# Kernel optimization log

Measured on AMD Instinct MI355X. Metric: run time of the kernel, lower is better.

Reference implementation:

```python
import jax, jax.numpy as jnp
import numpy as np

NUM_HEADS = 16
HEAD_DIM = 64  # latent_dim // num_heads = 1024 // 16


def setup_inputs() -> dict:
    key = jax.random.key(0)
    k1, k2, k3, k4 = jax.random.split(key, 4)
    B, S, C = 4, 2048, 1024
    x = jax.random.normal(k1, (B, S, C), dtype=jnp.float32)
    # torch nn.Linear weight layout: [out_features, in_features]
    W_qkv = jax.random.normal(k2, (2 * 1024 + C, C), dtype=jnp.float32) * (C ** -0.5)
    W_out = jax.random.normal(k3, (C, C), dtype=jnp.float32) * (C ** -0.5)
    b_out = jax.random.normal(k4, (C,), dtype=jnp.float32) * 0.01
    return {"x": x, "W_qkv": W_qkv, "W_out": W_out, "b_out": b_out}


def reference(x, W_qkv, W_out, b_out):
    B, S, C = x.shape
    H, CH = NUM_HEADS, HEAD_DIM
    qkv = jnp.einsum('bsc,oc->bso', x, W_qkv)          # [B, S, 2*latent + C]
    qkv = qkv.reshape(B, S, H, -1)                      # per-head: [CH, CH, C//H]
    q = qkv[..., :CH]
    k = qkv[..., CH:2 * CH]
    v = qkv[..., 2 * CH:]
    energy = jnp.einsum('bqhc,bkhc->bhqk', q, k)        # full score matrix
    scale = jnp.asarray(C, x.dtype) ** 0.5              # note: original scales by sqrt(C), not sqrt(head_dim)
    attn = jax.nn.softmax(energy / scale, axis=-1)
    out = jnp.einsum('bhqk,bkhc->bqhc', attn, v).reshape(B, S, -1)
    out = jnp.einsum('bsc,oc->bso', out, W_out) + b_out
    return out + x
```

## Files before the change

kernel.cpp:

```cpp
#include <hip/hip_runtime.h>
#include <hip/hip_bf16.h>
#include <stdint.h>

#define BB 4
#define SS 2048
#define CC 1024
#define HH 16
#define DD 64
#define MTOT (BB*SS)
#define NQKV 3072

typedef __attribute__((ext_vector_type(8))) short short8;
typedef __attribute__((ext_vector_type(4))) float f32x4;

#define MFMA16(A,B,C) __builtin_amdgcn_mfma_f32_16x16x32_bf16((A),(B),(C),0,0,0)
#define BARRIER() asm volatile("s_barrier" ::: "memory")

__device__ __forceinline__ ushort f2bf(float f) {
  uint32_t u = __builtin_bit_cast(uint32_t, f);
  u += 0x7FFFu + ((u >> 16) & 1u);
  return (ushort)(u >> 16);
}

__device__ __forceinline__ float bf2f(ushort u) {
  return __builtin_bit_cast(float, (uint32_t)u << 16);
}

__device__ __forceinline__ unsigned cvtpk(float lo, float hi) {
  unsigned r;
  asm("v_cvt_pk_bf16_f32 %0, %1, %2" : "=v"(r) : "v"(lo), "v"(hi));
  return r;
}

__device__ __forceinline__ float hw_exp2(float x) {
  float r;
  asm("v_exp_f32 %0, %1" : "=v"(r) : "v"(x));
  return r;
}

__global__ void cvt3_kernel(const float* __restrict__ a, ushort* __restrict__ da, int na4,
                            const float* __restrict__ b, ushort* __restrict__ db, int nb4,
                            const float* __restrict__ c, ushort* __restrict__ dc, int nc4) {
  int total = na4 + nb4 + nc4;
  int stride = gridDim.x * blockDim.x;
  for (int i = blockIdx.x * blockDim.x + threadIdx.x; i < total; i += stride) {
    const float4* s; ushort4* d; int k;
    if (i < na4)            { s = (const float4*)a; d = (ushort4*)da; k = i; }
    else if (i < na4 + nb4) { s = (const float4*)b; d = (ushort4*)db; k = i - na4; }
    else                    { s = (const float4*)c; d = (ushort4*)dc; k = i - na4 - nb4; }
    float4 v = s[k];
    ushort4 o;
    o.x = f2bf(v.x); o.y = f2bf(v.y); o.z = f2bf(v.z); o.w = f2bf(v.w);
    d[k] = o;
  }
}

__device__ __forceinline__ void stage_half128(const ushort* __restrict__ gsrc, ushort* ldsbase, int tid) {
  #pragma unroll
  for (int ld = 0; ld < 4; ++ld) {
    int ci = ld * 256 + tid;
    int row = ci >> 3, slot = ci & 7;
    const ushort* src = gsrc + (size_t)row * 1024 + ((slot ^ (row & 7)) << 3);
    __builtin_amdgcn_global_load_lds(
        (const __attribute__((address_space(1))) uint32_t*)src,
        (__attribute__((address_space(3))) uint32_t*)(ldsbase + ci * 8), 16, 0, 0);
  }
}

__device__ __forceinline__ short8 rd_frag(const ushort* Lb, int row, int slot) {
  return *(const short8*)(Lb + row * 64 + ((slot ^ (row & 7)) << 3));
}

__device__ __forceinline__ void core128(const ushort* __restrict__ A, const ushort* __restrict__ Bw,
                                        int m0, int n0, ushort* L, f32x4 acc[4][4]) {
  const int tid = threadIdx.x, lane = tid & 63, w = tid >> 6;
  const int q = lane & 15, g = lane >> 4;
  const int wm = (w >> 1) * 64, wn = (w & 1) * 64;
  const ushort* Ag = A + (size_t)m0 * 1024;
  const ushort* Bg = Bw + (size_t)n0 * 1024;

  #pragma unroll
  for (int tt = 0; tt < 2; ++tt) {
    stage_half128(Ag + tt * 64, L + tt * 16384, tid);
    stage_half128(Bg + tt * 64, L + tt * 16384 + 8192, tid);
  }
  asm volatile("s_waitcnt vmcnt(8)" ::: "memory");
  BARRIER();

  #pragma unroll 1
  for (int t = 0; t < 16; ++t) {
    const ushort* La = L + (t & 1) * 16384;
    const ushort* Lb = La + 8192;
    short8 af[4][2], bf[4][2];
    #pragma unroll
    for (int mi = 0; mi < 4; ++mi)
      #pragma unroll
      for (int ks = 0; ks < 2; ++ks)
        af[mi][ks] = rd_frag(La, wm + mi * 16 + q, ks * 4 + g);
    #pragma unroll
    for (int nj = 0; nj < 4; ++nj)
      #pragma unroll
      for (int ks = 0; ks < 2; ++ks)
        bf[nj][ks] = rd_frag(Lb, wn + nj * 16 + q, ks * 4 + g);
    #pragma unroll
    for (int mi = 0; mi < 4; ++mi)
      #pragma unroll
      for (int nj = 0; nj < 4; ++nj) {
        acc[mi][nj] = MFMA16(af[mi][0], bf[nj][0], acc[mi][nj]);
        acc[mi][nj] = MFMA16(af[mi][1], bf[nj][1], acc[mi][nj]);
      }
    BARRIER();
    if (t <= 13) {
      ushort* Ls = L + (t & 1) * 16384;
      stage_half128(Ag + (t + 2) * 64, Ls, tid);
      stage_half128(Bg + (t + 2) * 64, Ls + 8192, tid);
      asm volatile("s_waitcnt vmcnt(8)" ::: "memory");
      BARRIER();
    } else if (t == 14) {
      asm volatile("s_waitcnt vmcnt(0)" ::: "memory");
      BARRIER();
    }
  }
}

__global__ __launch_bounds__(256, 2) void gemm_qkv(const ushort* __restrict__ xb, const ushort* __restrict__ wqkv,
                                                   ushort* __restrict__ qfbuf, ushort* __restrict__ kfbuf,
                                                   ushort* __restrict__ vfbuf) {
  __shared__ __align__(16) ushort L[32768];
  const int bid = blockIdx.x;
  const int xcd = bid & 7, r0 = bid >> 3;
  const int m0 = (r0 / 3) * 128, n0 = (xcd * 3 + (r0 % 3)) * 128;

  f32x4 acc[4][4];
  #pragma unroll
  for (int i = 0; i < 4; ++i)
    #pragma unroll
    for (int j = 0; j < 4; ++j) acc[i][j] = f32x4{0.f, 0.f, 0.f, 0.f};
  core128(xb, wqkv, m0, n0, L, acc);

  const int lane = threadIdx.x & 63, wave = threadIdx.x >> 6;
  const int g = lane >> 4, q = lane & 15;
  const int wm = (wave >> 1) * 64, wn = (wave & 1) * 64;
  const int s0 = m0 & 2047, bb = m0 >> 11;

  #pragma unroll
  for (int j = 0; j < 4; ++j) {
    int n = n0 + wn + j * 16 + q;
    int h = n / 192;
    int which = (n - h * 192) >> 6;
    float scl = (which == 0) ? 0.045084222f : 1.0f;
    int nc = wn + j * 16 + q;
    #pragma unroll
    for (int i = 0; i < 4; ++i) {
      #pragma unroll
      for (int rr = 0; rr < 4; ++rr) {
        int mr = wm + i * 16 + g * 4 + rr;
        L[mr * 128 + (nc ^ ((mr & 7) << 4))] = f2bf(acc[i][j][rr] * scl);
      }
    }
  }
  __syncthreads();

  {
    const int n_g = n0 + wave * 32;
    const int h = n_g / 192, rem = n_g - h * 192, which = rem >> 6;
    const int bh = bb * 16 + h;
    if (which < 2) {
      ushort* dst0 = (which == 0) ? qfbuf : kfbuf;
      const int c0 = (rem & 63) >> 5;
      #pragma unroll
      for (int k = 0; k < 8; ++k) {
        int jt = (s0 >> 4) + k;
        int mr = k * 16 + (lane & 15);
        int nc0 = wave * 32 + (lane >> 4) * 8;
        short8 v = *(const short8*)(L + mr * 128 + (nc0 ^ ((mr & 7) << 4)));
        *(short8*)(dst0 + ((((size_t)bh * 128 + jt) * 2 + c0) * 64 + lane) * 8) = v;
      }
    } else {
      const int ct0 = (rem & 63) >> 4;
      #pragma unroll
      for (int k = 0; k < 8; ++k) {
        int jcr = k >> 1, ct = ct0 + (k & 1);
        int nc = wave * 32 + (k & 1) * 16 + (lane & 15);
        int mrb = jcr * 32 + (lane >> 4) * 8;
        short8 v;
        #pragma unroll
        for (int e = 0; e < 8; ++e) {
          int mr = mrb + e;
          v[e] = (short)L[mr * 128 + (nc ^ ((mr & 7) << 4))];
        }
        int jc = (s0 >> 5) + jcr;
        *(short8*)(vfbuf + ((((size_t)bh * 64 + jc) * 4 + ct) * 64 + lane) * 8) = v;
      }
    }
  }
}

__global__ __launch_bounds__(256, 2) void gemm_out(const ushort* __restrict__ ab, const ushort* __restrict__ wout,
                                                   const ushort* __restrict__ xbb, const float* __restrict__ bias,
                                                   float* __restrict__ out) {
  __shared__ __align__(16) ushort L[32768];
  const int bid = blockIdx.x;
  const int sw = (bid & 7) * 64 + (bid >> 3);
  const int m0 = (sw & 63) * 128, n0 = (sw >> 6) * 128;

  f32x4 acc[4][4];
  #pragma unroll
  for (int i = 0; i < 4; ++i)
    #pragma unroll
    for (int j = 0; j < 4; ++j) acc[i][j] = f32x4{0.f, 0.f, 0.f, 0.f};
  core128(ab, wout, m0, n0, L, acc);

  const int tid = threadIdx.x;
  const int lane = tid & 63, wave = tid >> 6;
  const int g = lane >> 4, q = lane & 15;
  const int wm = (wave >> 1) * 64, wn = (wave & 1) * 64;
  float* Lf = reinterpret_cast<float*>(L);

  #pragma unroll
  for (int j = 0; j < 4; ++j) {
    int nc = wn + j * 16 + q;
    #pragma unroll
    for (int i = 0; i < 4; ++i) {
      #pragma unroll
      for (int rr = 0; rr < 4; ++rr) {
        int mr = wm + i * 16 + g * 4 + rr;
        int swz = ((mr & 4) << 0) | ((mr & 8) << 1);
        Lf[mr * 128 + (nc ^ swz)] = acc[i][j][rr];
      }
    }
  }
  __syncthreads();

  #pragma unroll
  for (int k = 0; k < 16; ++k) {
    int ci = k * 256 + tid;
    int row = ci >> 5, cb = (ci & 31) * 4;
    int swz = ((row & 4) << 0) | ((row & 8) << 1);
    float4 v = *(const float4*)(Lf + row * 128 + (cb ^ swz));
    size_t m = (size_t)(m0 + row);
    int n = n0 + cb;
    ushort4 xr = *(const ushort4*)(xbb + m * 1024 + n);
    float4 bv = *(const float4*)(bias + n);
    float4 o;
    o.x = v.x + bv.x + bf2f(xr.x);
    o.y = v.y + bv.y + bf2f(xr.y);
    o.z = v.z + bv.z + bf2f(xr.z);
    o.w = v.w + bv.w + bf2f(xr.w);
    *(float4*)(out + m * 1024 + n) = o;
  }
}

__global__ __launch_bounds__(256) void attn_kernel(const ushort* __restrict__ QF, const ushort* __restrict__ KF,
                                                   const ushort* __restrict__ VF, ushort* __restrict__ aout) {
  __shared__ ushort Ps[4][16 * 72];
  const int bid = blockIdx.x;
  const int xcd = bid & 7, r = bid >> 3;
  const int qb = r & 31, bh = xcd + (r >> 5) * 8;
  const int lane = threadIdx.x & 63, wave = threadIdx.x >> 6;
  const int g = lane >> 4, q = lane & 15;
  const int qt = qb * 4 + wave;
  const f32x4 zed = {0.f, 0.f, 0.f, 0.f};

  const ushort* Qb = QF + (size_t)bh * 131072 + lane * 8;
  const ushort* Kp = KF + (size_t)bh * 131072 + lane * 8;
  const ushort* Vp = VF + (size_t)bh * 131072 + lane * 8;
  ushort* pw = Ps[wave];

  short8 onesf;
  #pragma unroll
  for (int e = 0; e < 8; ++e) onesf[e] = (short)0x3F80;

  short8 qf[2];
  #pragma unroll
  for (int c0 = 0; c0 < 2; ++c0)
    qf[c0] = *(const short8*)(Qb + ((size_t)qt * 2 + c0) * 512);

  f32x4 oa[4], la;
  la = zed;
  #pragma unroll
  for (int ct = 0; ct < 4; ++ct) oa[ct] = zed;

  #pragma unroll 1
  for (int j0 = 0; j0 < SS; j0 += 32) {
    const int jt0 = j0 >> 4, jc = j0 >> 5;
    short8 kf[2][2], vf[4];
    #pragma unroll
    for (int jj = 0; jj < 2; ++jj)
      #pragma unroll
      for (int c0 = 0; c0 < 2; ++c0)
        kf[jj][c0] = *(const short8*)(Kp + ((size_t)(jt0 + jj) * 2 + c0) * 512);
    #pragma unroll
    for (int ct = 0; ct < 4; ++ct)
      vf[ct] = *(const short8*)(Vp + ((size_t)jc * 4 + ct) * 512);

    f32x4 sa[2];
    __builtin_amdgcn_s_setprio(1);
    #pragma unroll
    for (int jj = 0; jj < 2; ++jj) {
      sa[jj] = MFMA16(kf[jj][0], qf[0], zed);
      sa[jj] = MFMA16(kf[jj][1], qf[1], sa[jj]);
    }
    __builtin_amdgcn_s_setprio(0);
    #pragma unroll
    for (int jj = 0; jj < 2; ++jj) {
      uint2 wv;
      wv.x = cvtpk(hw_exp2(sa[jj][0]), hw_exp2(sa[jj][1]));
      wv.y = cvtpk(hw_exp2(sa[jj][2]), hw_exp2(sa[jj][3]));
      *reinterpret_cast<uint2*>(pw + q * 72 + jj * 16 + 4 * g) = wv;
    }
    short8 pa = *reinterpret_cast<const short8*>(pw + q * 72 + g * 8);
    __builtin_amdgcn_s_setprio(1);
    #pragma unroll
    for (int ct = 0; ct < 4; ++ct)
      oa[ct] = MFMA16(pa, vf[ct], oa[ct]);
    la = MFMA16(pa, onesf, la);
    __builtin_amdgcn_s_setprio(0);
  }

  const int b = bh >> 4, h = bh & 15;
  float inv[4];
  #pragma unroll
  for (int r2 = 0; r2 < 4; ++r2) inv[r2] = 1.0f / la[r2];
  #pragma unroll
  for (int ct = 0; ct < 4; ++ct) {
    size_t rowb = (size_t)b * SS + qt * 16 + 4 * g;
    int col = h * DD + ct * 16 + q;
    aout[(rowb + 0) * CC + col] = f2bf(oa[ct][0] * inv[0]);
    aout[(rowb + 1) * CC + col] = f2bf(oa[ct][1] * inv[1]);
    aout[(rowb + 2) * CC + col] = f2bf(oa[ct][2] * inv[2]);
    aout[(rowb + 3) * CC + col] = f2bf(oa[ct][3] * inv[3]);
  }
}

extern "C" void kernel_launch(void* const* d_in, const int* in_sizes, int n_in,
                              void* d_out, int out_size, void* d_ws, size_t ws_size,
                              hipStream_t stream) {
  const float* x    = (const float*)d_in[0];
  const float* wqkv = (const float*)d_in[1];
  const float* wout = (const float*)d_in[2];
  const float* bias = (const float*)d_in[3];
  float* out = (float*)d_out;

  ushort* xb    = (ushort*)d_ws;
  ushort* wqkvb = xb + (size_t)8 * 1024 * 1024;
  ushort* woutb = wqkvb + (size_t)3 * 1024 * 1024;
  ushort* qfbuf = woutb + (size_t)1024 * 1024;
  ushort* kfbuf = qfbuf + (size_t)8 * 1024 * 1024;
  ushort* vfbuf = kfbuf + (size_t)8 * 1024 * 1024;
  ushort* aout  = vfbuf + (size_t)8 * 1024 * 1024;

  hipLaunchKernelGGL(cvt3_kernel, dim3(2048), dim3(256), 0, stream,
                     x, xb, 8 * 1024 * 1024 / 4,
                     wqkv, wqkvb, 3 * 1024 * 1024 / 4,
                     wout, woutb, 1024 * 1024 / 4);

  hipLaunchKernelGGL(gemm_qkv, dim3(1536), dim3(256), 0, stream,
                     xb, wqkvb, qfbuf, kfbuf, vfbuf);
  hipLaunchKernelGGL(attn_kernel, dim3(2048), dim3(256), 0, stream,
                     qfbuf, kfbuf, vfbuf, aout);
  hipLaunchKernelGGL(gemm_out, dim3(512), dim3(256), 0, stream,
                     aout, woutb, xb, bias, out);
}
```

Measured before the change: 222.1 us.

## Switch attention to 32x32 MFMA tiles with register-shuffled P and K prefetch

The attention kernel now has each wave own 32 query rows and computes scores and PV with 32x32x16 bf16 MFMAs instead of 16x16x32. The P tile is rearranged across lane halves with cross-lane shuffles rather than a round trip through shared memory, and the next K block is loaded one iteration ahead. The grid is halved to 1024 blocks. The aim is more work per wave and per K/V fragment load, with no LDS traffic for P, at the cost of more registers and fewer resident waves.

```diff
diff --git a/kernel.cpp b/kernel.cpp
--- a/kernel.cpp
+++ b/kernel.cpp
@@ -12,8 +12,11 @@
 
 typedef __attribute__((ext_vector_type(8))) short short8;
 typedef __attribute__((ext_vector_type(4))) float f32x4;
+typedef __attribute__((ext_vector_type(16))) float f32x16;
+typedef __attribute__((ext_vector_type(4))) unsigned uint4v;
 
 #define MFMA16(A,B,C) __builtin_amdgcn_mfma_f32_16x16x32_bf16((A),(B),(C),0,0,0)
+#define MFMA32(A,B,C) __builtin_amdgcn_mfma_f32_32x32x16_bf16((A),(B),(C),0,0,0)
 #define BARRIER() asm volatile("s_barrier" ::: "memory")
 
 __device__ __forceinline__ ushort f2bf(float f) {
@@ -36,6 +39,13 @@
   float r;
   asm("v_exp_f32 %0, %1" : "=v"(r) : "v"(x));
   return r;
+}
+
+__device__ __forceinline__ f32x16 zero16() {
+  f32x16 v;
+  #pragma unroll
+  for (int i = 0; i < 16; ++i) v[i] = 0.f;
+  return v;
 }
 
 __global__ void cvt3_kernel(const float* __restrict__ a, ushort* __restrict__ da, int na4,
@@ -253,83 +263,99 @@
 
 __global__ __launch_bounds__(256) void attn_kernel(const ushort* __restrict__ QF, const ushort* __restrict__ KF,
                                                    const ushort* __restrict__ VF, ushort* __restrict__ aout) {
-  __shared__ ushort Ps[4][16 * 72];
   const int bid = blockIdx.x;
   const int xcd = bid & 7, r = bid >> 3;
-  const int qb = r & 31, bh = xcd + (r >> 5) * 8;
+  const int qb = r & 15, bh = xcd + (r >> 4) * 8;
   const int lane = threadIdx.x & 63, wave = threadIdx.x >> 6;
-  const int g = lane >> 4, q = lane & 15;
+  const int l31 = lane & 31, hi = lane >> 5, l15 = lane & 15, l31h = l31 >> 4;
   const int qt = qb * 4 + wave;
-  const f32x4 zed = {0.f, 0.f, 0.f, 0.f};
-
-  const ushort* Qb = QF + (size_t)bh * 131072 + lane * 8;
-  const ushort* Kp = KF + (size_t)bh * 131072 + lane * 8;
-  const ushort* Vp = VF + (size_t)bh * 131072 + lane * 8;
-  ushort* pw = Ps[wave];
+
+  const ushort* QFb = QF + (size_t)bh * 131072;
+  const ushort* KFb = KF + (size_t)bh * 131072;
+  const ushort* VFb = VF + (size_t)bh * 131072;
 
   short8 onesf;
   #pragma unroll
   for (int e = 0; e < 8; ++e) onesf[e] = (short)0x3F80;
 
-  short8 qf[2];
-  #pragma unroll
-  for (int c0 = 0; c0 < 2; ++c0)
-    qf[c0] = *(const short8*)(Qb + ((size_t)qt * 2 + c0) * 512);
-
-  f32x4 oa[4], la;
-  la = zed;
-  #pragma unroll
-  for (int ct = 0; ct < 4; ++ct) oa[ct] = zed;
+  short8 qf[4];
+  #pragma unroll
+  for (int kc = 0; kc < 4; ++kc) {
+    int jt16 = qt * 2 + l31h;
+    int lane2 = (((kc * 2 + hi) & 3) << 4) + l15;
+    qf[kc] = *(const short8*)(QFb + ((size_t)(jt16 * 2 + (kc >> 1)) * 64 + lane2) * 8);
+  }
+
+  f32x16 oa0 = zero16(), oa1 = zero16(), la = zero16();
+
+  short8 kfA[4], kfB[4], vf[2][2];
+  #pragma unroll
+  for (int kc = 0; kc < 4; ++kc) {
+    int lane2 = (((kc * 2 + hi) & 3) << 4) + l15;
+    kfA[kc] = *(const short8*)(KFb + ((size_t)(l31h * 2 + (kc >> 1)) * 64 + lane2) * 8);
+  }
 
   #pragma unroll 1
   for (int j0 = 0; j0 < SS; j0 += 32) {
-    const int jt0 = j0 >> 4, jc = j0 >> 5;
-    short8 kf[2][2], vf[4];
-    #pragma unroll
-    for (int jj = 0; jj < 2; ++jj)
-      #pragma unroll
-      for (int c0 = 0; c0 < 2; ++c0)
-        kf[jj][c0] = *(const short8*)(Kp + ((size_t)(jt0 + jj) * 2 + c0) * 512);
-    #pragma unroll
-    for (int ct = 0; ct < 4; ++ct)
-      vf[ct] = *(const short8*)(Vp + ((size_t)jc * 4 + ct) * 512);
-
-    f32x4 sa[2];
+    #pragma unroll
+    for (int kj = 0; kj < 2; ++kj)
+      #pragma unroll
+      for (int cb = 0; cb < 2; ++cb) {
+        int ct = cb * 2 + l31h;
+        int lane16 = (((kj * 2 + hi) & 3) << 4) + l15;
+        vf[kj][cb] = *(const short8*)(VFb + ((size_t)((j0 >> 5) * 4 + ct) * 64 + lane16) * 8);
+      }
+    if (j0 + 32 < SS) {
+      #pragma unroll
+      for (int kc = 0; kc < 4; ++kc) {
+        int jt16 = ((j0 + 32) >> 4) + l31h;
+        int lane2 = (((kc * 2 + hi) & 3) << 4) + l15;
+        kfB[kc] = *(const short8*)(KFb + ((size_t)(jt16 * 2 + (kc >> 1)) * 64 + lane2) * 8);
+      }
+    }
+
+    f32x16 sa = zero16();
     __builtin_amdgcn_s_setprio(1);
     #pragma unroll
-    for (int jj = 0; jj < 2; ++jj) {
-      sa[jj] = MFMA16(kf[jj][0], qf[0], zed);
-      sa[jj] = MFMA16(kf[jj][1], qf[1], sa[jj]);
-    }
+    for (int kc = 0; kc < 4; ++kc) sa = MFMA32(kfA[kc], qf[kc], sa);
     __builtin_amdgcn_s_setprio(0);
-    #pragma unroll
-    for (int jj = 0; jj < 2; ++jj) {
-      uint2 wv;
-      wv.x = cvtpk(hw_exp2(sa[jj][0]), hw_exp2(sa[jj][1]));
-      wv.y = cvtpk(hw_exp2(sa[jj][2]), hw_exp2(sa[jj][3]));
-      *reinterpret_cast<uint2*>(pw + q * 72 + jj * 16 + 4 * g) = wv;
-    }
-    short8 pa = *reinterpret_cast<const short8*>(pw + q * 72 + g * 8);
-    __builtin_amdgcn_s_setprio(1);
-    #pragma unroll
-    for (int ct = 0; ct < 4; ++ct)
-      oa[ct] = MFMA16(pa, vf[ct], oa[ct]);
-    la = MFMA16(pa, onesf, la);
-    __builtin_amdgcn_s_setprio(0);
+
+    unsigned w[8];
+    #pragma unroll
+    for (int i = 0; i < 8; ++i)
+      w[i] = cvtpk(hw_exp2(sa[2 * i]), hw_exp2(sa[2 * i + 1]));
+
+    #pragma unroll
+    for (int kj = 0; kj < 2; ++kj) {
+      unsigned a0 = w[kj * 4 + 0], a1 = w[kj * 4 + 1];
+      unsigned b0 = w[kj * 4 + 2], b1 = w[kj * 4 + 3];
+      unsigned sa0 = __shfl_xor(a0, 32, 64), sa1 = __shfl_xor(a1, 32, 64);
+      unsigned sb0 = __shfl_xor(b0, 32, 64), sb1 = __shfl_xor(b1, 32, 64);
+      uint4v t;
+      t.x = hi ? sb0 : a0;
+      t.y = hi ? sb1 : a1;
+      t.z = hi ? b0 : sa0;
+      t.w = hi ? b1 : sa1;
+      short8 pa = __builtin_bit_cast(short8, t);
+      __builtin_amdgcn_s_setprio(1);
+      oa0 = MFMA32(pa, vf[kj][0], oa0);
+      oa1 = MFMA32(pa, vf[kj][1], oa1);
+      la  = MFMA32(pa, onesf, la);
+      __builtin_amdgcn_s_setprio(0);
+    }
+
+    #pragma unroll
+    for (int kc = 0; kc < 4; ++kc) kfA[kc] = kfB[kc];
   }
 
   const int b = bh >> 4, h = bh & 15;
-  float inv[4];
-  #pragma unroll
-  for (int r2 = 0; r2 < 4; ++r2) inv[r2] = 1.0f / la[r2];
-  #pragma unroll
-  for (int ct = 0; ct < 4; ++ct) {
-    size_t rowb = (size_t)b * SS + qt * 16 + 4 * g;
-    int col = h * DD + ct * 16 + q;
-    aout[(rowb + 0) * CC + col] = f2bf(oa[ct][0] * inv[0]);
-    aout[(rowb + 1) * CC + col] = f2bf(oa[ct][1] * inv[1]);
-    aout[(rowb + 2) * CC + col] = f2bf(oa[ct][2] * inv[2]);
-    aout[(rowb + 3) * CC + col] = f2bf(oa[ct][3] * inv[3]);
+  #pragma unroll
+  for (int r16 = 0; r16 < 16; ++r16) {
+    float inv = 1.0f / la[r16];
+    int row = qt * 32 + (r16 & 3) + 8 * (r16 >> 2) + 4 * hi;
+    size_t base = ((size_t)b * SS + row) * CC + h * DD;
+    aout[base + l31]      = f2bf(oa0[r16] * inv);
+    aout[base + 32 + l31] = f2bf(oa1[r16] * inv);
   }
 }
 
@@ -357,7 +383,7 @@
 
   hipLaunchKernelGGL(gemm_qkv, dim3(1536), dim3(256), 0, stream,
                      xb, wqkvb, qfbuf, kfbuf, vfbuf);
-  hipLaunchKernelGGL(attn_kernel, dim3(2048), dim3(256), 0, stream,
+  hipLaunchKernelGGL(attn_kernel, dim3(1024), dim3(256), 0, stream,
                      qfbuf, kfbuf, vfbuf, aout);
   hipLaunchKernelGGL(gemm_out, dim3(512), dim3(256), 0, stream,
                      aout, woutb, xb, bias, out);
```

After: 210.6 us. 5.2% less time.
